# Kernel optimization log

Hardware: AMD Instinct MI355X
Metric: run time of the kernel (lower is better)

The kernel has to match this reference:

```python
import jax, jax.numpy as jnp
import numpy as np

D_MODEL = 2048
N_HEADS = 16
D_HEAD = D_MODEL // N_HEADS


def setup_inputs() -> dict:
    key = jax.random.key(0)
    ks = jax.random.split(key, 9)
    s = 1.0 / np.sqrt(D_MODEL)
    x = jax.random.normal(ks[0], (2, 2048, D_MODEL), dtype=jnp.float32)
    wq = jax.random.uniform(ks[1], (D_MODEL, D_MODEL), jnp.float32, -s, s)
    wk = jax.random.uniform(ks[2], (D_MODEL, D_MODEL), jnp.float32, -s, s)
    wv = jax.random.uniform(ks[3], (D_MODEL, D_MODEL), jnp.float32, -s, s)
    wo = jax.random.uniform(ks[4], (D_MODEL, D_MODEL), jnp.float32, -s, s)
    bq = jax.random.uniform(ks[5], (D_MODEL,), jnp.float32, -s, s)
    bk = jax.random.uniform(ks[6], (D_MODEL,), jnp.float32, -s, s)
    bv = jax.random.uniform(ks[7], (D_MODEL,), jnp.float32, -s, s)
    bo = jax.random.uniform(ks[8], (D_MODEL,), jnp.float32, -s, s)
    return {"x": x, "wq": wq, "bq": bq, "wk": wk, "bk": bk,
            "wv": wv, "bv": bv, "wo": wo, "bo": bo}


def reference(x, wq, bq, wk, bk, wv, bv, wo, bo):
    b, s, _ = x.shape
    # torch Linear: y = x @ W.T + b
    q = (jnp.einsum('bsd,ed->bse', x, wq) + bq).reshape(b, s, N_HEADS, D_HEAD)
    k = (jnp.einsum('bsd,ed->bse', x, wk) + bk).reshape(b, s, N_HEADS, D_HEAD)
    v = (jnp.einsum('bsd,ed->bse', x, wv) + bv).reshape(b, s, N_HEADS, D_HEAD)
    scale = 1.0 / np.sqrt(D_HEAD).astype(np.float32)
    # [b, h, s, s] attention scores (naive full materialization, as in source)
    attn = jnp.einsum('bqhd,bkhd->bhqk', q, k) * scale
    attn = jax.nn.softmax(attn, axis=-1)
    out = jnp.einsum('bhqk,bkhd->bqhd', attn, v).reshape(b, s, D_MODEL)
    return jnp.einsum('bsd,ed->bse', out, wo) + bo
```

## Files before the change

### kernel.cpp

```cpp
#include <hip/hip_runtime.h>

#define D_MODEL 2048
#define SEQ     2048
#define NB      2
#define NH      16
#define DH      128
#define MROWS   (NB*SEQ)
#define GK      2048
#define NT      (GK/64)

typedef __bf16 bf16x8 __attribute__((ext_vector_type(8)));
typedef float  f32x4  __attribute__((ext_vector_type(4)));
typedef unsigned short ushort8 __attribute__((ext_vector_type(8)));
typedef unsigned int   u32x4   __attribute__((ext_vector_type(4)));

__device__ __forceinline__ unsigned short f2bf(float f) {
  unsigned int u = __float_as_uint(f);
  u += 0x7FFFu + ((u >> 16) & 1u);
  return (unsigned short)(u >> 16);
}

__device__ __forceinline__ unsigned int cvtpk_bf16(float lo, float hi) {
  unsigned int r;
  asm("v_cvt_pk_bf16_f32 %0, %1, %2" : "=v"(r) : "v"(lo), "v"(hi));
  return r;
}

__device__ __forceinline__ void gload16(void* lds, const void* g) {
  __builtin_amdgcn_global_load_lds(
      (__attribute__((address_space(1))) void*)(g),
      (__attribute__((address_space(3))) void*)(lds), 16, 0, 0);
}

__global__ __launch_bounds__(256) void cast_f32_bf16(
    const float* __restrict__ in, unsigned short* __restrict__ out) {
  int i = blockIdx.x * 256 + threadIdx.x;
  const float4* p = (const float4*)in;
  float4 a = p[2*i], b = p[2*i+1];
  ushort8 o;
  o[0]=f2bf(a.x); o[1]=f2bf(a.y); o[2]=f2bf(a.z); o[3]=f2bf(a.w);
  o[4]=f2bf(b.x); o[5]=f2bf(b.y); o[6]=f2bf(b.z); o[7]=f2bf(b.w);
  ((ushort8*)out)[i] = o;
}

__global__ __launch_bounds__(512, 2) void gemm256(
    const unsigned short* __restrict__ A,
    const unsigned short* __restrict__ B,
    const float* __restrict__ b0, const float* __restrict__ b1,
    const float* __restrict__ b2,
    unsigned short* __restrict__ qo, unsigned short* __restrict__ ko,
    unsigned short* __restrict__ vo, float* __restrict__ fo,
    int mode, int nblk)
{
  __shared__ char lds[3*49152];

  const int tid  = threadIdx.x;
  const int lane = tid & 63, wid = tid >> 6;
  const int la   = lane & 15, hi = lane >> 4;
  const int wm   = wid >> 2,  wn = wid & 3;

  const int linear = ((int)(blockIdx.x & 7)) * (nblk >> 3) + ((int)blockIdx.x >> 3);
  const int bm = linear & 31, bn = linear >> 5;

  const unsigned short* Ab = A + (size_t)(bm*128) * GK;
  const unsigned short* Bb = B + (size_t)(bn*256) * GK;

  f32x4 acc[4][4];
  #pragma unroll
  for (int m = 0; m < 4; m++)
    #pragma unroll
    for (int n = 0; n < 4; n++) acc[m][n] = f32x4{0.f,0.f,0.f,0.f};

#define STAGE(slot, kt) do {                                                  \
    int sb_ = (slot) * 49152;                                                 \
    _Pragma("unroll")                                                         \
    for (int j = 0; j < 2; j++) {                                             \
      int idx = j*512 + tid;                                                  \
      int row = idx >> 3;                                                     \
      int c   = (idx & 7) << 4;                                               \
      gload16(lds + sb_ + idx*16,                                             \
              Ab + (size_t)row*GK + (kt)*64 + ((c ^ ((row&7)<<4)) >> 1));     \
    }                                                                         \
    _Pragma("unroll")                                                         \
    for (int j = 0; j < 4; j++) {                                             \
      int idx = j*512 + tid;                                                  \
      int row = idx >> 3;                                                     \
      int c   = (idx & 7) << 4;                                               \
      gload16(lds + sb_ + 16384 + idx*16,                                     \
              Bb + (size_t)row*GK + (kt)*64 + ((c ^ ((row&7)<<4)) >> 1));     \
    }                                                                         \
  } while (0)

  STAGE(0, 0);
  STAGE(1, 1);

  int cs = 0, ps = 2;
  const int xr = (la & 7) << 4;

  #pragma unroll 1
  for (int t = 0; t < NT; ++t) {
    if (t + 2 < NT) STAGE(ps, t + 2);

    if (t + 2 < NT)      asm volatile("s_waitcnt vmcnt(12)" ::: "memory");
    else if (t + 1 < NT) asm volatile("s_waitcnt vmcnt(6)"  ::: "memory");
    else                 asm volatile("s_waitcnt vmcnt(0)"  ::: "memory");
    __builtin_amdgcn_s_barrier();
    asm volatile("" ::: "memory");

    const char* sa = lds + cs*49152;
    const char* sb = sa + 16384;
    #pragma unroll
    for (int ks = 0; ks < 2; ks++) {
      bf16x8 a[4], b[4];
      #pragma unroll
      for (int m = 0; m < 4; m++)
        a[m] = *(const bf16x8*)(sa + (((wm*64 + m*16 + la)*128 + ks*64 + hi*16) ^ xr));
      #pragma unroll
      for (int n = 0; n < 4; n++)
        b[n] = *(const bf16x8*)(sb + (((wn*64 + n*16 + la)*128 + ks*64 + hi*16) ^ xr));
      #pragma unroll
      for (int m = 0; m < 4; m++)
        #pragma unroll
        for (int n = 0; n < 4; n++)
          acc[m][n] = __builtin_amdgcn_mfma_f32_16x16x32_bf16(a[m], b[n], acc[m][n], 0, 0, 0);
    }
    asm volatile("" ::: "memory");
    __builtin_amdgcn_s_barrier();

    cs = cs + 1; if (cs == 3) cs = 0;
    ps = ps + 1; if (ps == 3) ps = 0;
  }
#undef STAGE

  const int row0 = bm*128 + wm*64;
  const int col0 = bn*256 + wn*64;

  if (mode == 1) {
    #pragma unroll
    for (int n = 0; n < 4; n++) {
      int col = col0 + n*16 + la;
      float bv = b0[col];
      #pragma unroll
      for (int m = 0; m < 4; m++)
        #pragma unroll
        for (int r = 0; r < 4; r++) {
          int row = row0 + m*16 + hi*4 + r;
          fo[(size_t)row*D_MODEL + col] = acc[m][n][r] + bv;
        }
    }
  } else {
    const int mat = col0 >> 11;
    const float* bp = (mat == 0) ? b0 : (mat == 1) ? b1 : b2;
    #pragma unroll
    for (int n = 0; n < 4; n++) {
      int col = col0 + n*16 + la;
      int c   = col & 2047;
      int h   = c >> 7, d = c & 127;
      float bv = bp[c];
      #pragma unroll
      for (int m = 0; m < 4; m++)
        #pragma unroll
        for (int r = 0; r < 4; r++) {
          int row = row0 + m*16 + hi*4 + r;
          int b   = row >> 11, s = row & (SEQ-1);
          unsigned short val = f2bf(acc[m][n][r] + bv);
          if (mat == 0) {
            qo[((size_t)(b*NH + h)*SEQ + s)*DH + d] = val;
          } else if (mat == 1) {
            size_t base = ((size_t)(b*NH + h)*SEQ + (size_t)(s >> 6)*64)*DH;
            int boff = (((s & 63) << 8) + (d << 1)) ^ ((s & 7) << 4);
            ko[base + (boff >> 1)] = val;
          } else {
            size_t base = ((size_t)(b*NH + h)*SEQ + (size_t)(s >> 6)*64)*DH;
            int boff = ((d << 7) + ((s & 63) << 1)) ^ ((d & 7) << 4);
            vo[base + (boff >> 1)] = val;
          }
        }
    }
  }
}

__global__ __launch_bounds__(256, 2) void attn_fwd(
    const unsigned short* __restrict__ Q,
    const unsigned short* __restrict__ Kg,
    const unsigned short* __restrict__ VTg,
    unsigned short* __restrict__ O)
{
  __shared__ unsigned short Ks [2][64*128];
  __shared__ unsigned short VTs[2][128*64];

  const int tid  = threadIdx.x;
  const int lane = tid & 63, wid = tid >> 6;
  const int la   = lane & 15, hi = lane >> 4;
  const int swz  = ((int)(blockIdx.x & 7) << 6) + ((int)blockIdx.x >> 3);
  const int bh   = swz >> 4;
  const int q0   = (swz & 15) << 7;
  const int b    = bh >> 4, h = bh & 15;

  const unsigned short* Qh = Q   + (size_t)bh * SEQ * DH;
  const unsigned short* Kh = Kg  + (size_t)bh * SEQ * DH;
  const unsigned short* Vh = VTg + (size_t)bh * SEQ * DH;

  const int qrow = q0 + wid * 32;

  bf16x8 qf[2][4];
  #pragma unroll
  for (int qi = 0; qi < 2; qi++)
    #pragma unroll
    for (int ks = 0; ks < 4; ks++)
      qf[qi][ks] = *(const bf16x8*)(Qh + (size_t)(qrow + qi*16 + la)*DH + ks*32 + hi*8);

  f32x4 o[2][8];
  float mrun[2], lrun[2];
  #pragma unroll
  for (int qi = 0; qi < 2; qi++) {
    #pragma unroll
    for (int df = 0; df < 8; df++) o[qi][df] = f32x4{0.f,0.f,0.f,0.f};
    mrun[qi] = -1e30f; lrun[qi] = 0.f;
  }

  #pragma unroll
  for (int i = 0; i < 4; i++) {
    int off = i*4096 + tid*16;
    gload16((char*)Ks[0]  + off, (const char*)Kh + off);
    gload16((char*)VTs[0] + off, (const char*)Vh + off);
  }
  __syncthreads();

  const float sc = 0.08838834764831845f;

  #pragma unroll 1
  for (int t = 0; t < SEQ/64; ++t) {
    const int cur = t & 1;

    if (t + 1 < SEQ/64) {
      const char* kt = (const char*)(Kh + (size_t)(t+1)*(64*DH));
      const char* vt = (const char*)(Vh + (size_t)(t+1)*(64*DH));
      #pragma unroll
      for (int i = 0; i < 4; i++) {
        int off = i*4096 + tid*16;
        gload16((char*)Ks[cur^1]  + off, kt + off);
        gload16((char*)VTs[cur^1] + off, vt + off);
      }
    }

    f32x4 S[4][2];
    #pragma unroll
    for (int mf = 0; mf < 4; mf++)
      #pragma unroll
      for (int qi = 0; qi < 2; qi++) S[mf][qi] = f32x4{0.f,0.f,0.f,0.f};
    #pragma unroll
    for (int ks = 0; ks < 4; ks++) {
      bf16x8 kf[4];
      #pragma unroll
      for (int mf = 0; mf < 4; mf++) {
        int boff = (((mf*16 + la) << 8) + (ks << 6) + (hi << 4)) ^ ((la & 7) << 4);
        kf[mf] = *(const bf16x8*)((const char*)Ks[cur] + boff);
      }
      #pragma unroll
      for (int mf = 0; mf < 4; mf++)
        #pragma unroll
        for (int qi = 0; qi < 2; qi++)
          S[mf][qi] = __builtin_amdgcn_mfma_f32_16x16x32_bf16(kf[mf], qf[qi][ks], S[mf][qi], 0, 0, 0);
    }

    unsigned int pf[2][2][4];
    #pragma unroll
    for (int qi = 0; qi < 2; qi++) {
      float pm = S[0][qi][0];
      #pragma unroll
      for (int mf = 0; mf < 4; mf++)
        #pragma unroll
        for (int r = 0; r < 4; r++) pm = fmaxf(pm, S[mf][qi][r]);
      pm = fmaxf(pm, __shfl_xor(pm, 16));
      pm = fmaxf(pm, __shfl_xor(pm, 32));
      pm *= sc;
      float mn    = fmaxf(mrun[qi], pm);
      float alpha = __expf(mrun[qi] - mn);
      mrun[qi] = mn;

      float p[4][4]; float rs = 0.f;
      #pragma unroll
      for (int mf = 0; mf < 4; mf++)
        #pragma unroll
        for (int r = 0; r < 4; r++) {
          float e = __expf(fmaf(S[mf][qi][r], sc, -mn));
          p[mf][r] = e; rs += e;
        }
      rs += __shfl_xor(rs, 16);
      rs += __shfl_xor(rs, 32);
      lrun[qi] = lrun[qi]*alpha + rs;

      #pragma unroll
      for (int r = 0; r < 4; r++) {
        float ar = __shfl(alpha, (lane & 48) | ((hi << 2) | r), 64);
        #pragma unroll
        for (int df = 0; df < 8; df++) o[qi][df][r] *= ar;
      }

      unsigned int c[4][2];
      #pragma unroll
      for (int mf = 0; mf < 4; mf++) {
        c[mf][0] = cvtpk_bf16(p[mf][0], p[mf][1]);
        c[mf][1] = cvtpk_bf16(p[mf][2], p[mf][3]);
      }
      #pragma unroll
      for (int ks2 = 0; ks2 < 2; ks2++) {
        #pragma unroll
        for (int w = 0; w < 4; w++) {
          int src = la + 16*(2*(hi & 1) + (w >> 1));
          unsigned int t0 = __shfl(c[2*ks2    ][w & 1], src, 64);
          unsigned int t1 = __shfl(c[2*ks2 + 1][w & 1], src, 64);
          pf[qi][ks2][w] = (hi >> 1) ? t1 : t0;
        }
      }
    }

    #pragma unroll
    for (int ks2 = 0; ks2 < 2; ks2++) {
      #pragma unroll
      for (int df = 0; df < 8; df++) {
        int vrow = df*16 + la;
        int boff = ((vrow << 7) + (ks2 << 6) + (hi << 4)) ^ ((la & 7) << 4);
        bf16x8 vf = *(const bf16x8*)((const char*)VTs[cur] + boff);
        #pragma unroll
        for (int qi = 0; qi < 2; qi++) {
          u32x4 pw = {pf[qi][ks2][0], pf[qi][ks2][1], pf[qi][ks2][2], pf[qi][ks2][3]};
          o[qi][df] = __builtin_amdgcn_mfma_f32_16x16x32_bf16(
              __builtin_bit_cast(bf16x8, pw), vf, o[qi][df], 0, 0, 0);
        }
      }
    }
    __syncthreads();
  }

  unsigned short* Ob = O + (size_t)b * SEQ * D_MODEL + h * DH;
  #pragma unroll
  for (int qi = 0; qi < 2; qi++) {
    float linv[4];
    #pragma unroll
    for (int r = 0; r < 4; r++)
      linv[r] = 1.0f / __shfl(lrun[qi], (lane & 48) | ((hi << 2) | r), 64);
    #pragma unroll
    for (int df = 0; df < 8; df++)
      #pragma unroll
      for (int r = 0; r < 4; r++) {
        int srow = qrow + qi*16 + hi*4 + r;
        Ob[(size_t)srow * D_MODEL + df*16 + la] = f2bf(o[qi][df][r] * linv[r]);
      }
  }
}

extern "C" void kernel_launch(void* const* d_in, const int* in_sizes, int n_in,
                              void* d_out, int out_size, void* d_ws, size_t ws_size,
                              hipStream_t stream) {
  const float* x  = (const float*)d_in[0];
  const float* wq = (const float*)d_in[1];
  const float* bq = (const float*)d_in[2];
  const float* wk = (const float*)d_in[3];
  const float* bk = (const float*)d_in[4];
  const float* wv = (const float*)d_in[5];
  const float* bv = (const float*)d_in[6];
  const float* wo = (const float*)d_in[7];
  const float* bo = (const float*)d_in[8];
  float* out = (float*)d_out;

  const size_t X = (size_t)MROWS * D_MODEL;
  const size_t W = (size_t)D_MODEL * D_MODEL;

  unsigned short* ws  = (unsigned short*)d_ws;
  unsigned short* xb  = ws;
  unsigned short* wqb = xb  + X;
  unsigned short* wkb = wqb + W;
  unsigned short* wvb = wkb + W;
  unsigned short* wob = wvb + W;
  unsigned short* qb  = wob + W;
  unsigned short* kb  = qb  + X;
  unsigned short* vtg = kb  + X;
  unsigned short* ab  = vtg + X;

  cast_f32_bf16<<<dim3((unsigned)(X/2048)), 256, 0, stream>>>(x,  xb);
  cast_f32_bf16<<<dim3((unsigned)(W/2048)), 256, 0, stream>>>(wq, wqb);
  cast_f32_bf16<<<dim3((unsigned)(W/2048)), 256, 0, stream>>>(wk, wkb);
  cast_f32_bf16<<<dim3((unsigned)(W/2048)), 256, 0, stream>>>(wv, wvb);
  cast_f32_bf16<<<dim3((unsigned)(W/2048)), 256, 0, stream>>>(wo, wob);

  gemm256<<<dim3(768), 512, 0, stream>>>(xb, wqb, bq, bk, bv,
                                         qb, kb, vtg, nullptr, 0, 768);

  attn_fwd<<<dim3(512), 256, 0, stream>>>(qb, kb, vtg, ab);

  gemm256<<<dim3(256), 512, 0, stream>>>(ab, wob, bo, bo, bo,
                                         nullptr, nullptr, nullptr, out, 1, 256);
}
```

Before: 302.4 us.

## Split GEMM main loop into two phases interleaving global loads with MFMA

```diff
diff --git a/kernel.cpp b/kernel.cpp
--- a/kernel.cpp
+++ b/kernel.cpp
@@ -71,7 +71,7 @@
     #pragma unroll
     for (int n = 0; n < 4; n++) acc[m][n] = f32x4{0.f,0.f,0.f,0.f};
 
-#define STAGE(slot, kt) do {                                                  \
+#define STAGE_A(slot, kt) do {                                                \
     int sb_ = (slot) * 49152;                                                 \
     _Pragma("unroll")                                                         \
     for (int j = 0; j < 2; j++) {                                             \
@@ -81,6 +81,10 @@
       gload16(lds + sb_ + idx*16,                                             \
               Ab + (size_t)row*GK + (kt)*64 + ((c ^ ((row&7)<<4)) >> 1));     \
     }                                                                         \
+  } while (0)
+
+#define STAGE_B(slot, kt) do {                                                \
+    int sb_ = (slot) * 49152;                                                 \
     _Pragma("unroll")                                                         \
     for (int j = 0; j < 4; j++) {                                             \
       int idx = j*512 + tid;                                                  \
@@ -91,46 +95,74 @@
     }                                                                         \
   } while (0)
 
-  STAGE(0, 0);
-  STAGE(1, 1);
+  STAGE_A(0, 0); STAGE_B(0, 0);
+  STAGE_A(1, 1); STAGE_B(1, 1);
 
   int cs = 0, ps = 2;
   const int xr = (la & 7) << 4;
 
   #pragma unroll 1
   for (int t = 0; t < NT; ++t) {
-    if (t + 2 < NT) STAGE(ps, t + 2);
-
-    if (t + 2 < NT)      asm volatile("s_waitcnt vmcnt(12)" ::: "memory");
-    else if (t + 1 < NT) asm volatile("s_waitcnt vmcnt(6)"  ::: "memory");
-    else                 asm volatile("s_waitcnt vmcnt(0)"  ::: "memory");
+    if (t + 1 < NT) asm volatile("s_waitcnt vmcnt(6)" ::: "memory");
+    else            asm volatile("s_waitcnt vmcnt(0)" ::: "memory");
     __builtin_amdgcn_s_barrier();
-    asm volatile("" ::: "memory");
-
-    const char* sa = lds + cs*49152;
-    const char* sb = sa + 16384;
-    #pragma unroll
-    for (int ks = 0; ks < 2; ks++) {
-      bf16x8 a[4], b[4];
-      #pragma unroll
-      for (int m = 0; m < 4; m++)
-        a[m] = *(const bf16x8*)(sa + (((wm*64 + m*16 + la)*128 + ks*64 + hi*16) ^ xr));
+
+    const char* sa  = lds + cs*49152;
+    const char* sbp = sa + 16384;
+
+    bf16x8 bfr[4][2], aA[2][2];
+    #pragma unroll
+    for (int n = 0; n < 4; n++)
+      #pragma unroll
+      for (int ks = 0; ks < 2; ks++)
+        bfr[n][ks] = *(const bf16x8*)(sbp + (((wn*64 + n*16 + la)*128 + ks*64 + hi*16) ^ xr));
+    #pragma unroll
+    for (int m = 0; m < 2; m++)
+      #pragma unroll
+      for (int ks = 0; ks < 2; ks++)
+        aA[m][ks] = *(const bf16x8*)(sa + (((wm*64 + m*16 + la)*128 + ks*64 + hi*16) ^ xr));
+
+    if (t + 2 < NT) STAGE_A(ps, t + 2);
+
+    asm volatile("s_waitcnt lgkmcnt(0)" ::: "memory");
+    __builtin_amdgcn_sched_barrier(0);
+    __builtin_amdgcn_s_setprio(1);
+    #pragma unroll
+    for (int m = 0; m < 2; m++)
       #pragma unroll
       for (int n = 0; n < 4; n++)
-        b[n] = *(const bf16x8*)(sb + (((wn*64 + n*16 + la)*128 + ks*64 + hi*16) ^ xr));
-      #pragma unroll
-      for (int m = 0; m < 4; m++)
-        #pragma unroll
-        for (int n = 0; n < 4; n++)
-          acc[m][n] = __builtin_amdgcn_mfma_f32_16x16x32_bf16(a[m], b[n], acc[m][n], 0, 0, 0);
-    }
-    asm volatile("" ::: "memory");
+        #pragma unroll
+        for (int ks = 0; ks < 2; ks++)
+          acc[m][n] = __builtin_amdgcn_mfma_f32_16x16x32_bf16(aA[m][ks], bfr[n][ks], acc[m][n], 0, 0, 0);
+    __builtin_amdgcn_s_setprio(0);
     __builtin_amdgcn_s_barrier();
+
+    bf16x8 aB[2][2];
+    #pragma unroll
+    for (int m = 0; m < 2; m++)
+      #pragma unroll
+      for (int ks = 0; ks < 2; ks++)
+        aB[m][ks] = *(const bf16x8*)(sa + (((wm*64 + (m+2)*16 + la)*128 + ks*64 + hi*16) ^ xr));
+
+    if (t + 2 < NT) STAGE_B(ps, t + 2);
+
+    asm volatile("s_waitcnt lgkmcnt(0)" ::: "memory");
+    __builtin_amdgcn_sched_barrier(0);
+    __builtin_amdgcn_s_setprio(1);
+    #pragma unroll
+    for (int m = 0; m < 2; m++)
+      #pragma unroll
+      for (int n = 0; n < 4; n++)
+        #pragma unroll
+        for (int ks = 0; ks < 2; ks++)
+          acc[m+2][n] = __builtin_amdgcn_mfma_f32_16x16x32_bf16(aB[m][ks], bfr[n][ks], acc[m+2][n], 0, 0, 0);
+    __builtin_amdgcn_s_setprio(0);
 
     cs = cs + 1; if (cs == 3) cs = 0;
     ps = ps + 1; if (ps == 3) ps = 0;
   }
-#undef STAGE
+#undef STAGE_A
+#undef STAGE_B
 
   const int row0 = bm*128 + wm*64;
   const int col0 = bn*256 + wn*64;
```

New measurement: 301.1 us. About the same (-0.4%).
